# Kernel optimization log

Measured on AMD Instinct MI355X. Metric: run time of the kernel, lower is better.

Reference implementation:

```python
import jax, jax.numpy as jnp
import numpy as np

USER_NUM = 100_000
ITEM_NUM = 50_000
N = USER_NUM + ITEM_NUM          # total nodes in the bipartite graph
HIDDEN = 64
LAYERS = 3
BATCH = 4096
NNZ = 4_800_000                  # ~avg degree 32


def setup_inputs() -> dict:
    key = jax.random.key(0)
    ks = jax.random.split(key, 7)
    emb = jax.random.normal(ks[0], (N, HIDDEN), dtype=jnp.float32) * 0.02
    rows = jax.random.randint(ks[1], (NNZ,), 0, N, dtype=jnp.int32)
    cols = jax.random.randint(ks[2], (NNZ,), 0, N, dtype=jnp.int32)
    # normalized-laplacian-like positive values, scaled ~ 1/avg_degree
    vals = jax.random.uniform(ks[3], (NNZ,), dtype=jnp.float32) * (1.0 / 32.0)
    user = jax.random.randint(ks[4], (BATCH,), 0, USER_NUM, dtype=jnp.int32)
    pos = jax.random.randint(ks[5], (BATCH,), USER_NUM, N, dtype=jnp.int32)
    neg = jax.random.randint(ks[6], (BATCH,), USER_NUM, N, dtype=jnp.int32)
    return {"emb": emb, "vals": vals, "rows": rows, "cols": cols,
            "user": user, "pos": pos, "neg": neg}


def _spmm(rows, cols, vals, x):
    # sparse [N,N] @ dense [N,d] in COO form: gather + scale + segment-sum
    return jax.ops.segment_sum(vals[:, None] * x[cols], rows, num_segments=N)


def reference(emb, vals, rows, cols, user, pos, neg):
    # layer-0 gathers
    user_acc = emb[user]
    pos_acc = emb[pos]
    neg_acc = emb[neg]
    e = emb
    for _ in range(LAYERS):
        e = _spmm(rows, cols, vals, e)
        user_acc = user_acc + e[user]
        pos_acc = pos_acc + e[pos]
        neg_acc = neg_acc + e[neg]
    denom = jnp.float32(LAYERS + 1)
    u = user_acc / denom   # mean over stacked layers
    p = pos_acc / denom
    n = neg_acc / denom
    pos_logits = jnp.einsum('id,id->i', u, p)
    neg_logits = jnp.einsum('id,id->i', u, n)
    # -log(sigmoid(x)) == -log_sigmoid(x) (numerically stable)
    loss = -jax.nn.log_sigmoid(pos_logits - neg_logits)
    return loss.sum()
```

## Files before the change

### kernel.cpp

```cpp
#include <hip/hip_runtime.h>

#define HIDDEN 64
#define PAD 96
#define CHUNK 8192
#define NBMAX 640
#define CAP 9600
#define S_SCALE 64.0f
#define INV_S 0.015625f

typedef unsigned int uint;
typedef unsigned char uchar;

__device__ __forceinline__ ushort f2bf(float f) {
    uint u = __float_as_uint(f);
    u = (u + 0x7FFFu + ((u >> 16) & 1u)) >> 16;
    return (ushort)u;
}
__device__ __forceinline__ float bf2f(ushort h) {
    return __uint_as_float(((uint)h) << 16);
}

#if __has_builtin(__builtin_amdgcn_cvt_pk_fp8_f32) && __has_builtin(__builtin_amdgcn_cvt_pk_f32_fp8)
#define FP8_HW 1
#else
#define FP8_HW 0
#endif

__device__ __forceinline__ uint enc8(float a, float b, float c, float d) {
#if FP8_HW
    int r = __builtin_amdgcn_cvt_pk_fp8_f32(a, b, 0, false);
    r = __builtin_amdgcn_cvt_pk_fp8_f32(c, d, r, true);
    return (uint)r;
#else
    auto enc1 = [](float x) -> uint {
        uint u = __float_as_uint(x);
        uint s = (u >> 24) & 0x80u;
        float af = fabsf(x);
        if (af < 0.015625f) return s;
        if (af >= 448.f) return s | 0x7Eu;
        uint bits = u & 0x7FFFFFFFu;
        bits -= (120u << 23);
        uint r = (bits + 0x7FFFFu + ((bits >> 20) & 1u)) >> 20;
        if (r > 0x7Eu) r = 0x7Eu;
        return s | r;
    };
    return enc1(a) | (enc1(b) << 8) | (enc1(c) << 16) | (enc1(d) << 24);
#endif
}

__device__ __forceinline__ float4 dec8(uint u) {
#if FP8_HW
    auto lo = __builtin_amdgcn_cvt_pk_f32_fp8((int)u, false);
    auto hi = __builtin_amdgcn_cvt_pk_f32_fp8((int)u, true);
    return make_float4(lo[0], lo[1], hi[0], hi[1]);
#else
    auto dec1 = [](uint b) -> float {
        uint m = b & 0x7Fu;
        uint s = (b & 0x80u) << 24;
        uint bits = m ? (s | ((m + 960u) << 20)) : s;
        return __uint_as_float(bits);
    };
    return make_float4(dec1(u & 0xFF), dec1((u >> 8) & 0xFF),
                       dec1((u >> 16) & 0xFF), dec1((u >> 24) & 0xFF));
#endif
}


__global__ void __launch_bounds__(256) k_f2fp8(const float4* __restrict__ src,
                                               uint2* __restrict__ dst, int n8) {
    int i = blockIdx.x * blockDim.x + threadIdx.x;
    if (i >= n8) return;
    float4 f0 = src[2 * i], f1 = src[2 * i + 1];
    uint2 o;
    o.x = enc8(f0.x * S_SCALE, f0.y * S_SCALE, f0.z * S_SCALE, f0.w * S_SCALE);
    o.y = enc8(f1.x * S_SCALE, f1.y * S_SCALE, f1.z * S_SCALE, f1.w * S_SCALE);
    dst[i] = o;
}


__global__ void __launch_bounds__(1024) k_stage(const int* __restrict__ rows,
                                                const int* __restrict__ cols,
                                                const float* __restrict__ vals,
                                                int* __restrict__ cursor,
                                                uint* __restrict__ smeta,
                                                ushort* __restrict__ sval,
                                                int nnz, int nb) {
    __shared__ int    hS[NBMAX];
    __shared__ int    lsS[NBMAX];
    __shared__ int    gsS[NBMAX];
    __shared__ int    lcS[NBMAX];
    __shared__ int    ps[1024];
    __shared__ uint   stgm[CHUNK];
    __shared__ ushort stgv[CHUNK];

    int t  = threadIdx.x;
    int cb = blockIdx.x * CHUNK;

    for (int k = t; k < nb; k += 1024) hS[k] = 0;
    __syncthreads();

    int4 ra[2];
    #pragma unroll
    for (int j = 0; j < 2; ++j) {
        int idx = cb + j * 4096 + t * 4;
        int4 r4;
        if (idx + 3 < nnz) {
            r4 = *(const int4*)(rows + idx);
        } else {
            r4.x = (idx     < nnz) ? rows[idx]     : -1;
            r4.y = (idx + 1 < nnz) ? rows[idx + 1] : -1;
            r4.z = (idx + 2 < nnz) ? rows[idx + 2] : -1;
            r4.w = (idx + 3 < nnz) ? rows[idx + 3] : -1;
        }
        ra[j] = r4;
        if (r4.x >= 0) atomicAdd(&hS[r4.x >> 8], 1);
        if (r4.y >= 0) atomicAdd(&hS[r4.y >> 8], 1);
        if (r4.z >= 0) atomicAdd(&hS[r4.z >> 8], 1);
        if (r4.w >= 0) atomicAdd(&hS[r4.w >> 8], 1);
    }
    __syncthreads();

    int k0 = 2 * t, k1 = 2 * t + 1;
    int c0 = (k0 < nb) ? hS[k0] : 0;
    int c1 = (k1 < nb) ? hS[k1] : 0;
    ps[t] = c0 + c1;
    __syncthreads();
    for (int d = 1; d < 1024; d <<= 1) {
        int p = (t >= d) ? ps[t - d] : 0;
        __syncthreads();
        ps[t] += p;
        __syncthreads();
    }
    int excl = ps[t] - (c0 + c1);
    if (k0 < nb) { lsS[k0] = excl;      gsS[k0] = atomicAdd(&cursor[k0], c0); }
    if (k1 < nb) { lsS[k1] = excl + c0; gsS[k1] = atomicAdd(&cursor[k1], c1); }
    __syncthreads();
    for (int k = t; k < nb; k += 1024) lcS[k] = lsS[k];
    __syncthreads();

    #pragma unroll
    for (int j = 0; j < 2; ++j) {
        int idx = cb + j * 4096 + t * 4;
        int4 r4 = ra[j];
        int4 c4; float4 v4;
        if (idx + 3 < nnz) {
            c4 = *(const int4*)(cols + idx);
            v4 = *(const float4*)(vals + idx);
        } else {
            c4.x = (idx     < nnz) ? cols[idx]     : 0;
            c4.y = (idx + 1 < nnz) ? cols[idx + 1] : 0;
            c4.z = (idx + 2 < nnz) ? cols[idx + 2] : 0;
            c4.w = (idx + 3 < nnz) ? cols[idx + 3] : 0;
            v4.x = (idx     < nnz) ? vals[idx]     : 0.f;
            v4.y = (idx + 1 < nnz) ? vals[idx + 1] : 0.f;
            v4.z = (idx + 2 < nnz) ? vals[idx + 2] : 0.f;
            v4.w = (idx + 3 < nnz) ? vals[idx + 3] : 0.f;
        }
        if (r4.x >= 0) { int s = atomicAdd(&lcS[r4.x >> 8], 1);
            stgm[s] = (uint)c4.x | ((uint)(r4.x & 255) << 18); stgv[s] = f2bf(v4.x); }
        if (r4.y >= 0) { int s = atomicAdd(&lcS[r4.y >> 8], 1);
            stgm[s] = (uint)c4.y | ((uint)(r4.y & 255) << 18); stgv[s] = f2bf(v4.y); }
        if (r4.z >= 0) { int s = atomicAdd(&lcS[r4.z >> 8], 1);
            stgm[s] = (uint)c4.z | ((uint)(r4.z & 255) << 18); stgv[s] = f2bf(v4.z); }
        if (r4.w >= 0) { int s = atomicAdd(&lcS[r4.w >> 8], 1);
            stgm[s] = (uint)c4.w | ((uint)(r4.w & 255) << 18); stgv[s] = f2bf(v4.w); }
    }
    __syncthreads();

    int m_total = nnz - cb; if (m_total > CHUNK) m_total = CHUNK;
    for (int i = t; i < m_total; i += 1024) {
        int lo = 0, hi = nb - 1;
        while (lo < hi) {
            int mid = (lo + hi + 1) >> 1;
            if (lsS[mid] <= i) lo = mid; else hi = mid - 1;
        }
        int k = lo;
        int pos = gsS[k] + (i - lsS[k]);
        if (pos < CAP) {
            smeta[(size_t)k * CAP + pos] = stgm[i];
            sval [(size_t)k * CAP + pos] = stgv[i];
        }
    }
}

__global__ void __launch_bounds__(1024) k_fine(const uint* __restrict__ smeta,
                                               const ushort* __restrict__ sval,
                                               const int* __restrict__ stagecnt,
                                               int* __restrict__ cols_ell,
                                               ushort* __restrict__ vals_ell,
                                               int* __restrict__ cnt, int n) {
    __shared__ uint   out_m[CAP];
    __shared__ ushort out_v[CAP];
    __shared__ int hist[256], rstart[256], cursor[256], s2[256];
    int k = blockIdx.x;
    int t = threadIdx.x;
    size_t s0 = (size_t)k * CAP;
    int ck = stagecnt[k]; if (ck > CAP) ck = CAP;
    if (t < 256) hist[t] = 0;
    __syncthreads();
    for (int i = t; i < ck; i += 1024)
        atomicAdd(&hist[smeta[s0 + i] >> 18], 1);
    __syncthreads();
    if (t < 256) s2[t] = hist[t];
    __syncthreads();
    for (int d = 1; d < 256; d <<= 1) {
        int p = (t < 256 && t >= d) ? s2[t - d] : 0;
        __syncthreads();
        if (t < 256) s2[t] += p;
        __syncthreads();
    }
    if (t < 256) {
        int rs = s2[t] - hist[t];
        rstart[t] = rs;
        cursor[t] = rs;
        int row = (k << 8) + t;
        if (row < n) cnt[row] = hist[t];
    }
    __syncthreads();
    for (int i = t; i < ck; i += 1024) {
        uint m = smeta[s0 + i];
        ushort v = sval[s0 + i];
        int lr = (int)(m >> 18);
        int slot = atomicAdd(&cursor[lr], 1);
        if (slot < CAP) { out_m[slot] = m & 0x3FFFFu; out_v[slot] = v; }
    }
    __syncthreads();
    for (int idx = t; idx < 256 * PAD; idx += 1024) {
        int lr = idx / PAD, j = idx - lr * PAD;
        if (j < hist[lr]) {
            int row = (k << 8) + lr;
            cols_ell[(size_t)row * PAD + j] = (int)out_m[rstart[lr] + j];
            vals_ell[(size_t)row * PAD + j] = out_v[rstart[lr] + j];
        }
    }
}


__device__ __forceinline__ float4 spmm_row4(const int* __restrict__ cnt,
                                            const int* __restrict__ cols_ell,
                                            const ushort* __restrict__ vals_ell,
                                            const uchar* __restrict__ x,
                                            int row, int lane) {
    int len = cnt[row]; if (len > PAD) len = PAD;
    const int*    cbp = cols_ell + (size_t)row * PAD;
    const ushort* vbp = vals_ell + (size_t)row * PAD;
    int g4 = (lane & 15) * 4;
    int e = lane >> 4;
    float a0 = 0.f, a1 = 0.f, a2 = 0.f, a3 = 0.f;
    float b0 = 0.f, b1 = 0.f, b2 = 0.f, b3 = 0.f;
    for (int j0 = 0; j0 < len; j0 += 64) {
        int m = len - j0; if (m > 64) m = 64;
        int c = 0; float v = 0.f;
        if (lane < m) {
            c = cbp[j0 + lane];
            v = bf2f(vbp[j0 + lane]);
        }
        int steps = (m + 3) >> 2;
        int s = 0;
        for (; s + 3 < steps; s += 4) {
            int i0 = 4 * s + e, i1 = i0 + 4, i2 = i0 + 8, i3 = i0 + 12;
            int   c0 = __shfl(c, i0); int   c1 = __shfl(c, i1);
            int   c2 = __shfl(c, i2); int   c3 = __shfl(c, i3);
            float v0 = __shfl(v, i0); float v1 = __shfl(v, i1);
            float v2 = __shfl(v, i2); float v3 = __shfl(v, i3);
            uint u0 = *(const uint*)(x + ((size_t)c0 << 6) + g4);
            uint u1 = *(const uint*)(x + ((size_t)c1 << 6) + g4);
            uint u2 = *(const uint*)(x + ((size_t)c2 << 6) + g4);
            uint u3 = *(const uint*)(x + ((size_t)c3 << 6) + g4);
            float4 x0 = dec8(u0); float4 x1 = dec8(u1);
            float4 x2 = dec8(u2); float4 x3 = dec8(u3);
            a0 += v0 * x0.x; a1 += v0 * x0.y; a2 += v0 * x0.z; a3 += v0 * x0.w;
            b0 += v1 * x1.x; b1 += v1 * x1.y; b2 += v1 * x1.z; b3 += v1 * x1.w;
            a0 += v2 * x2.x; a1 += v2 * x2.y; a2 += v2 * x2.z; a3 += v2 * x2.w;
            b0 += v3 * x3.x; b1 += v3 * x3.y; b2 += v3 * x3.z; b3 += v3 * x3.w;
        }
        for (; s < steps; ++s) {
            int i0 = 4 * s + e;
            int c0 = __shfl(c, i0); float v0 = __shfl(v, i0);
            uint u0 = *(const uint*)(x + ((size_t)c0 << 6) + g4);
            float4 x0 = dec8(u0);
            a0 += v0 * x0.x; a1 += v0 * x0.y; a2 += v0 * x0.z; a3 += v0 * x0.w;
        }
    }
    a0 += b0; a1 += b1; a2 += b2; a3 += b3;
    a0 += __shfl_xor(a0, 16); a1 += __shfl_xor(a1, 16);
    a2 += __shfl_xor(a2, 16); a3 += __shfl_xor(a3, 16);
    a0 += __shfl_xor(a0, 32); a1 += __shfl_xor(a1, 32);
    a2 += __shfl_xor(a2, 32); a3 += __shfl_xor(a3, 32);
    return make_float4(a0, a1, a2, a3);
}

__global__ void __launch_bounds__(256) k_spmm(const int* __restrict__ cnt,
                                              const int* __restrict__ cols_ell,
                                              const ushort* __restrict__ vals_ell,
                                              const uchar* __restrict__ x,
                                              uchar* __restrict__ y, int n) {
    int row  = (int)((blockIdx.x * blockDim.x + threadIdx.x) >> 6);
    int lane = threadIdx.x & 63;
    if (row >= n) return;
    float4 a = spmm_row4(cnt, cols_ell, vals_ell, x, row, lane);
    if (lane < 16) {
        uint r = enc8(a.x, a.y, a.z, a.w);
        *(uint*)(y + ((size_t)row << 6) + lane * 4) = r;
    }
}

__global__ void __launch_bounds__(256) k_spmm_batch(const int* __restrict__ cnt,
                                                    const int* __restrict__ cols_ell,
                                                    const ushort* __restrict__ vals_ell,
                                                    const uchar* __restrict__ x,
                                                    const int* __restrict__ user,
                                                    const int* __restrict__ pos,
                                                    const int* __restrict__ neg,
                                                    int batch, float* __restrict__ acc) {
    int slot = (int)((blockIdx.x * blockDim.x + threadIdx.x) >> 6);
    int lane = threadIdx.x & 63;
    if (slot >= 3 * batch) return;
    int which = slot / batch, i = slot - which * batch;
    const int* sel = (which == 0) ? user : (which == 1 ? pos : neg);
    float4 a = spmm_row4(cnt, cols_ell, vals_ell, x, sel[i], lane);
    if (lane < 16) {
        float4* p = (float4*)(acc + (size_t)slot * HIDDEN + lane * 4);
        float4 old = *p;
        old.x += a.x * INV_S; old.y += a.y * INV_S;
        old.z += a.z * INV_S; old.w += a.w * INV_S;
        *p = old;
    }
}


__global__ void __launch_bounds__(256) k_gather0(const float* __restrict__ e,
                                                 const int* __restrict__ user,
                                                 const int* __restrict__ pos,
                                                 const int* __restrict__ neg,
                                                 int batch, float* __restrict__ acc) {
    int row  = (int)((blockIdx.x * blockDim.x + threadIdx.x) >> 6);
    int lane = threadIdx.x & 63;
    if (row >= 3 * batch) return;
    int which = row / batch, i = row - which * batch;
    const int* sel = (which == 0) ? user : (which == 1 ? pos : neg);
    int s = sel[i];
    acc[(size_t)row * HIDDEN + lane] = e[(size_t)s * HIDDEN + lane];
}

__global__ void __launch_bounds__(256) k_gather8(const uchar* __restrict__ e,
                                                 const int* __restrict__ user,
                                                 const int* __restrict__ pos,
                                                 const int* __restrict__ neg,
                                                 int batch, float* __restrict__ acc) {
    int t    = blockIdx.x * blockDim.x + threadIdx.x;
    int wv   = t >> 6;
    int lane = threadIdx.x & 63;
    int row  = wv * 4 + (lane >> 4);
    if (row >= 3 * batch) return;
    int which = row / batch, i = row - which * batch;
    const int* sel = (which == 0) ? user : (which == 1 ? pos : neg);
    int s = sel[i];
    int g4 = (lane & 15) * 4;
    uint u = *(const uint*)(e + ((size_t)s << 6) + g4);
    float4 d = dec8(u);
    float4* p = (float4*)(acc + (size_t)row * HIDDEN + g4);
    float4 old = *p;
    old.x += d.x * INV_S; old.y += d.y * INV_S;
    old.z += d.z * INV_S; old.w += d.w * INV_S;
    *p = old;
}


__global__ void __launch_bounds__(256) k_loss(const float* __restrict__ acc, int batch,
                                              float* __restrict__ out) {
    int i    = (int)((blockIdx.x * blockDim.x + threadIdx.x) >> 6);
    int lane = threadIdx.x & 63;
    if (i >= batch) return;
    float u  = acc[(size_t)i * HIDDEN + lane] * 0.25f;
    float p  = acc[(size_t)(i + batch) * HIDDEN + lane] * 0.25f;
    float nn = acc[(size_t)(i + 2 * batch) * HIDDEN + lane] * 0.25f;
    float sp = u * p, sn = u * nn;
    for (int d = 32; d > 0; d >>= 1) {
        sp += __shfl_down(sp, d);
        sn += __shfl_down(sn, d);
    }
    if (lane == 0) {
        float z = sn - sp;
        float loss = fmaxf(z, 0.f) + log1pf(expf(-fabsf(z)));
        atomicAdd(out, loss);
    }
}


extern "C" void kernel_launch(void* const* d_in, const int* in_sizes, int n_in,
                              void* d_out, int out_size, void* d_ws, size_t ws_size,
                              hipStream_t stream) {
    (void)n_in; (void)out_size; (void)ws_size;
    const float* emb  = (const float*)d_in[0];
    const float* vals = (const float*)d_in[1];
    const int*   rows = (const int*)d_in[2];
    const int*   cols = (const int*)d_in[3];
    const int*   user = (const int*)d_in[4];
    const int*   pos  = (const int*)d_in[5];
    const int*   neg  = (const int*)d_in[6];

    const int n     = in_sizes[0] / HIDDEN;
    const int nnz   = in_sizes[1];
    const int batch = in_sizes[4];

    const int nb   = (n + 255) >> 8;
    const int nblk = (nnz + CHUNK - 1) / CHUNK;

    auto align256 = [](size_t x) { return (x + 255) & ~(size_t)255; };
    char* w = (char*)d_ws;
    int*    cnt      = (int*)w;    w += align256(sizeof(int)    * (size_t)n);
    int*    cursor   = (int*)w;    w += align256(sizeof(int)    * (size_t)NBMAX);
    int*    cols_ell = (int*)w;    w += align256(sizeof(int)    * (size_t)n * PAD);
    ushort* vals_ell = (ushort*)w; w += align256(sizeof(ushort) * (size_t)n * PAD);
    uchar*  emb8     = (uchar*)w;  w += align256((size_t)n * HIDDEN);
    uchar*  e0       = (uchar*)w;  w += align256((size_t)n * HIDDEN);
    uchar*  e1       = (uchar*)w;  w += align256((size_t)n * HIDDEN);
    float*  acc      = (float*)w;  w += align256(sizeof(float)  * (size_t)3 * batch * HIDDEN);
    uint*   smeta    = (uint*)w;   w += align256(sizeof(uint)   * (size_t)nb * CAP);
    ushort* sval     = (ushort*)w; w += align256(sizeof(ushort) * (size_t)nb * CAP);

    float* out = (float*)d_out;

    const int B = 256;
    dim3 blk(B);
    int g_conv = (n * HIDDEN / 8 + B - 1) / B;
    int g_spmm = (n + 3) / 4;
    int g_gath = (3 * batch + 3) / 4;
    int g_g8   = ((3 * batch + 3) / 4 * 64 + B - 1) / B;
    int g_loss = (batch + 3) / 4;

    hipMemsetAsync(cursor, 0, sizeof(int) * (size_t)NBMAX, stream);
    k_stage<<<nblk, 1024, 0, stream>>>(rows, cols, vals, cursor, smeta, sval, nnz, nb);
    k_fine<<<nb, 1024, 0, stream>>>(smeta, sval, cursor, cols_ell, vals_ell, cnt, n);

    k_f2fp8<<<g_conv, blk, 0, stream>>>((const float4*)emb, (uint2*)emb8, n * HIDDEN / 8);

    hipMemsetAsync(out, 0, sizeof(float), stream);

    k_gather0<<<g_gath, blk, 0, stream>>>(emb, user, pos, neg, batch, acc);
    k_spmm<<<g_spmm, blk, 0, stream>>>(cnt, cols_ell, vals_ell, emb8, e0, n);
    k_gather8<<<g_g8, blk, 0, stream>>>(e0, user, pos, neg, batch, acc);
    k_spmm<<<g_spmm, blk, 0, stream>>>(cnt, cols_ell, vals_ell, e0, e1, n);
    k_gather8<<<g_g8, blk, 0, stream>>>(e1, user, pos, neg, batch, acc);
    k_spmm_batch<<<g_gath, blk, 0, stream>>>(cnt, cols_ell, vals_ell, e1, user, pos, neg, batch, acc);

    k_loss<<<g_loss, blk, 0, stream>>>(acc, batch, out);
}
```

Measured before the change: 304.7 us.

## Pack ELL column and value into one word and split SpMM rows by halves

The staging kernel records each entry's bucket index in shared memory, which replaces the per-element binary search during scatter. The ELL format now packs an 18-bit column and a 14-bit truncated bf16 value into a single uint, padded to multiples of 16. This removes the separate value array and the shuffle-based broadcast in the SpMM inner loop. SpMM now gives each wave half of the 64 hidden features for a row, with lanes splitting entries eight ways, and blocks are ordered so both halves of the same rows run close together. Values lose two more mantissa bits, and each row's index list is read by two waves instead of one.

```diff
diff --git a/kernel.cpp b/kernel.cpp
--- a/kernel.cpp
+++ b/kernel.cpp
@@ -92,6 +92,7 @@
     __shared__ int    ps[1024];
     __shared__ uint   stgm[CHUNK];
     __shared__ ushort stgv[CHUNK];
+    __shared__ ushort stgb[CHUNK];
 
     int t  = threadIdx.x;
     int cb = blockIdx.x * CHUNK;
@@ -156,25 +157,20 @@
             v4.z = (idx + 2 < nnz) ? vals[idx + 2] : 0.f;
             v4.w = (idx + 3 < nnz) ? vals[idx + 3] : 0.f;
         }
-        if (r4.x >= 0) { int s = atomicAdd(&lcS[r4.x >> 8], 1);
-            stgm[s] = (uint)c4.x | ((uint)(r4.x & 255) << 18); stgv[s] = f2bf(v4.x); }
-        if (r4.y >= 0) { int s = atomicAdd(&lcS[r4.y >> 8], 1);
-            stgm[s] = (uint)c4.y | ((uint)(r4.y & 255) << 18); stgv[s] = f2bf(v4.y); }
-        if (r4.z >= 0) { int s = atomicAdd(&lcS[r4.z >> 8], 1);
-            stgm[s] = (uint)c4.z | ((uint)(r4.z & 255) << 18); stgv[s] = f2bf(v4.z); }
-        if (r4.w >= 0) { int s = atomicAdd(&lcS[r4.w >> 8], 1);
-            stgm[s] = (uint)c4.w | ((uint)(r4.w & 255) << 18); stgv[s] = f2bf(v4.w); }
+        if (r4.x >= 0) { int k = r4.x >> 8; int s = atomicAdd(&lcS[k], 1);
+            stgm[s] = (uint)c4.x | ((uint)(r4.x & 255) << 18); stgv[s] = f2bf(v4.x); stgb[s] = (ushort)k; }
+        if (r4.y >= 0) { int k = r4.y >> 8; int s = atomicAdd(&lcS[k], 1);
+            stgm[s] = (uint)c4.y | ((uint)(r4.y & 255) << 18); stgv[s] = f2bf(v4.y); stgb[s] = (ushort)k; }
+        if (r4.z >= 0) { int k = r4.z >> 8; int s = atomicAdd(&lcS[k], 1);
+            stgm[s] = (uint)c4.z | ((uint)(r4.z & 255) << 18); stgv[s] = f2bf(v4.z); stgb[s] = (ushort)k; }
+        if (r4.w >= 0) { int k = r4.w >> 8; int s = atomicAdd(&lcS[k], 1);
+            stgm[s] = (uint)c4.w | ((uint)(r4.w & 255) << 18); stgv[s] = f2bf(v4.w); stgb[s] = (ushort)k; }
     }
     __syncthreads();
 
     int m_total = nnz - cb; if (m_total > CHUNK) m_total = CHUNK;
     for (int i = t; i < m_total; i += 1024) {
-        int lo = 0, hi = nb - 1;
-        while (lo < hi) {
-            int mid = (lo + hi + 1) >> 1;
-            if (lsS[mid] <= i) lo = mid; else hi = mid - 1;
-        }
-        int k = lo;
+        int k = stgb[i];
         int pos = gsS[k] + (i - lsS[k]);
         if (pos < CAP) {
             smeta[(size_t)k * CAP + pos] = stgm[i];
@@ -186,11 +182,9 @@
 __global__ void __launch_bounds__(1024) k_fine(const uint* __restrict__ smeta,
                                                const ushort* __restrict__ sval,
                                                const int* __restrict__ stagecnt,
-                                               int* __restrict__ cols_ell,
-                                               ushort* __restrict__ vals_ell,
+                                               uint* __restrict__ ell,
                                                int* __restrict__ cnt, int n) {
-    __shared__ uint   out_m[CAP];
-    __shared__ ushort out_v[CAP];
+    __shared__ uint out_m[CAP];
     __shared__ int hist[256], rstart[256], cursor[256], s2[256];
     int k = blockIdx.x;
     int t = threadIdx.x;
@@ -219,70 +213,57 @@
     __syncthreads();
     for (int i = t; i < ck; i += 1024) {
         uint m = smeta[s0 + i];
-        ushort v = sval[s0 + i];
+        uint v = (uint)sval[s0 + i];
         int lr = (int)(m >> 18);
         int slot = atomicAdd(&cursor[lr], 1);
-        if (slot < CAP) { out_m[slot] = m & 0x3FFFFu; out_v[slot] = v; }
+        uint v14 = (v + 2u) >> 2;
+        if (v14 > 0x3FFFu) v14 = 0x3FFFu;
+        if (slot < CAP) out_m[slot] = (m & 0x3FFFFu) | (v14 << 18);
     }
     __syncthreads();
     for (int idx = t; idx < 256 * PAD; idx += 1024) {
         int lr = idx / PAD, j = idx - lr * PAD;
-        if (j < hist[lr]) {
+        int cr = hist[lr];
+        int cr16 = (cr + 15) & ~15;
+        if (j < cr) {
             int row = (k << 8) + lr;
-            cols_ell[(size_t)row * PAD + j] = (int)out_m[rstart[lr] + j];
-            vals_ell[(size_t)row * PAD + j] = out_v[rstart[lr] + j];
+            ell[(size_t)row * PAD + j] = out_m[rstart[lr] + j];
+        } else if (j < cr16) {
+            int row = (k << 8) + lr;
+            ell[(size_t)row * PAD + j] = 0u;
         }
     }
 }
 
 
-__device__ __forceinline__ float4 spmm_row4(const int* __restrict__ cnt,
-                                            const int* __restrict__ cols_ell,
-                                            const ushort* __restrict__ vals_ell,
-                                            const uchar* __restrict__ x,
-                                            int row, int lane) {
+__device__ __forceinline__ float4 spmm_row_half(const int* __restrict__ cnt,
+                                                const uint* __restrict__ ell,
+                                                const uchar* __restrict__ x,
+                                                int row, int lane, int half) {
     int len = cnt[row]; if (len > PAD) len = PAD;
-    const int*    cbp = cols_ell + (size_t)row * PAD;
-    const ushort* vbp = vals_ell + (size_t)row * PAD;
-    int g4 = (lane & 15) * 4;
-    int e = lane >> 4;
+    int len16 = (len + 15) & ~15;
+    const uint* mbp = ell + (size_t)row * PAD;
+    int e  = lane >> 3;
+    int g4 = (lane & 7) * 4 + half * 32;
     float a0 = 0.f, a1 = 0.f, a2 = 0.f, a3 = 0.f;
     float b0 = 0.f, b1 = 0.f, b2 = 0.f, b3 = 0.f;
-    for (int j0 = 0; j0 < len; j0 += 64) {
-        int m = len - j0; if (m > 64) m = 64;
-        int c = 0; float v = 0.f;
-        if (lane < m) {
-            c = cbp[j0 + lane];
-            v = bf2f(vbp[j0 + lane]);
-        }
-        int steps = (m + 3) >> 2;
-        int s = 0;
-        for (; s + 3 < steps; s += 4) {
-            int i0 = 4 * s + e, i1 = i0 + 4, i2 = i0 + 8, i3 = i0 + 12;
-            int   c0 = __shfl(c, i0); int   c1 = __shfl(c, i1);
-            int   c2 = __shfl(c, i2); int   c3 = __shfl(c, i3);
-            float v0 = __shfl(v, i0); float v1 = __shfl(v, i1);
-            float v2 = __shfl(v, i2); float v3 = __shfl(v, i3);
-            uint u0 = *(const uint*)(x + ((size_t)c0 << 6) + g4);
-            uint u1 = *(const uint*)(x + ((size_t)c1 << 6) + g4);
-            uint u2 = *(const uint*)(x + ((size_t)c2 << 6) + g4);
-            uint u3 = *(const uint*)(x + ((size_t)c3 << 6) + g4);
-            float4 x0 = dec8(u0); float4 x1 = dec8(u1);
-            float4 x2 = dec8(u2); float4 x3 = dec8(u3);
-            a0 += v0 * x0.x; a1 += v0 * x0.y; a2 += v0 * x0.z; a3 += v0 * x0.w;
-            b0 += v1 * x1.x; b1 += v1 * x1.y; b2 += v1 * x1.z; b3 += v1 * x1.w;
-            a0 += v2 * x2.x; a1 += v2 * x2.y; a2 += v2 * x2.z; a3 += v2 * x2.w;
-            b0 += v3 * x3.x; b1 += v3 * x3.y; b2 += v3 * x3.z; b3 += v3 * x3.w;
-        }
-        for (; s < steps; ++s) {
-            int i0 = 4 * s + e;
-            int c0 = __shfl(c, i0); float v0 = __shfl(v, i0);
-            uint u0 = *(const uint*)(x + ((size_t)c0 << 6) + g4);
-            float4 x0 = dec8(u0);
-            a0 += v0 * x0.x; a1 += v0 * x0.y; a2 += v0 * x0.z; a3 += v0 * x0.w;
-        }
+    for (int j = 0; j < len16; j += 16) {
+        uint m0 = mbp[j + e];
+        uint m1 = mbp[j + 8 + e];
+        int   c0 = (int)(m0 & 0x3FFFFu);
+        int   c1 = (int)(m1 & 0x3FFFFu);
+        float v0 = bf2f((ushort)((m0 >> 18) << 2));
+        float v1 = bf2f((ushort)((m1 >> 18) << 2));
+        uint u0 = *(const uint*)(x + ((size_t)c0 << 6) + g4);
+        uint u1 = *(const uint*)(x + ((size_t)c1 << 6) + g4);
+        float4 x0 = dec8(u0);
+        float4 x1 = dec8(u1);
+        a0 += v0 * x0.x; a1 += v0 * x0.y; a2 += v0 * x0.z; a3 += v0 * x0.w;
+        b0 += v1 * x1.x; b1 += v1 * x1.y; b2 += v1 * x1.z; b3 += v1 * x1.w;
     }
     a0 += b0; a1 += b1; a2 += b2; a3 += b3;
+    a0 += __shfl_xor(a0, 8);  a1 += __shfl_xor(a1, 8);
+    a2 += __shfl_xor(a2, 8);  a3 += __shfl_xor(a3, 8);
     a0 += __shfl_xor(a0, 16); a1 += __shfl_xor(a1, 16);
     a2 += __shfl_xor(a2, 16); a3 += __shfl_xor(a3, 16);
     a0 += __shfl_xor(a0, 32); a1 += __shfl_xor(a1, 32);
@@ -291,36 +272,40 @@
 }
 
 __global__ void __launch_bounds__(256) k_spmm(const int* __restrict__ cnt,
-                                              const int* __restrict__ cols_ell,
-                                              const ushort* __restrict__ vals_ell,
+                                              const uint* __restrict__ ell,
                                               const uchar* __restrict__ x,
                                               uchar* __restrict__ y, int n) {
-    int row  = (int)((blockIdx.x * blockDim.x + threadIdx.x) >> 6);
+    int b = blockIdx.x;
+    int q = b >> 3, r = b & 7;
+    int half = r >> 2;
+    int row = (q * 4 + (r & 3)) * 4 + (int)(threadIdx.x >> 6);
     int lane = threadIdx.x & 63;
     if (row >= n) return;
-    float4 a = spmm_row4(cnt, cols_ell, vals_ell, x, row, lane);
-    if (lane < 16) {
-        uint r = enc8(a.x, a.y, a.z, a.w);
-        *(uint*)(y + ((size_t)row << 6) + lane * 4) = r;
+    float4 a = spmm_row_half(cnt, ell, x, row, lane, half);
+    if (lane < 8) {
+        uint o = enc8(a.x, a.y, a.z, a.w);
+        *(uint*)(y + ((size_t)row << 6) + half * 32 + lane * 4) = o;
     }
 }
 
 __global__ void __launch_bounds__(256) k_spmm_batch(const int* __restrict__ cnt,
-                                                    const int* __restrict__ cols_ell,
-                                                    const ushort* __restrict__ vals_ell,
+                                                    const uint* __restrict__ ell,
                                                     const uchar* __restrict__ x,
                                                     const int* __restrict__ user,
                                                     const int* __restrict__ pos,
                                                     const int* __restrict__ neg,
                                                     int batch, float* __restrict__ acc) {
-    int slot = (int)((blockIdx.x * blockDim.x + threadIdx.x) >> 6);
+    int b = blockIdx.x;
+    int q = b >> 3, r = b & 7;
+    int half = r >> 2;
+    int slot = (q * 4 + (r & 3)) * 4 + (int)(threadIdx.x >> 6);
     int lane = threadIdx.x & 63;
     if (slot >= 3 * batch) return;
     int which = slot / batch, i = slot - which * batch;
     const int* sel = (which == 0) ? user : (which == 1 ? pos : neg);
-    float4 a = spmm_row4(cnt, cols_ell, vals_ell, x, sel[i], lane);
-    if (lane < 16) {
-        float4* p = (float4*)(acc + (size_t)slot * HIDDEN + lane * 4);
+    float4 a = spmm_row_half(cnt, ell, x, sel[i], lane, half);
+    if (lane < 8) {
+        float4* p = (float4*)(acc + (size_t)slot * HIDDEN + half * 32 + lane * 4);
         float4 old = *p;
         old.x += a.x * INV_S; old.y += a.y * INV_S;
         old.z += a.z * INV_S; old.w += a.w * INV_S;
@@ -409,41 +394,44 @@
 
     auto align256 = [](size_t x) { return (x + 255) & ~(size_t)255; };
     char* w = (char*)d_ws;
-    int*    cnt      = (int*)w;    w += align256(sizeof(int)    * (size_t)n);
-    int*    cursor   = (int*)w;    w += align256(sizeof(int)    * (size_t)NBMAX);
-    int*    cols_ell = (int*)w;    w += align256(sizeof(int)    * (size_t)n * PAD);
-    ushort* vals_ell = (ushort*)w; w += align256(sizeof(ushort) * (size_t)n * PAD);
-    uchar*  emb8     = (uchar*)w;  w += align256((size_t)n * HIDDEN);
-    uchar*  e0       = (uchar*)w;  w += align256((size_t)n * HIDDEN);
-    uchar*  e1       = (uchar*)w;  w += align256((size_t)n * HIDDEN);
-    float*  acc      = (float*)w;  w += align256(sizeof(float)  * (size_t)3 * batch * HIDDEN);
-    uint*   smeta    = (uint*)w;   w += align256(sizeof(uint)   * (size_t)nb * CAP);
-    ushort* sval     = (ushort*)w; w += align256(sizeof(ushort) * (size_t)nb * CAP);
+    int*    cnt    = (int*)w;    w += align256(sizeof(int)    * (size_t)n);
+    int*    cursor = (int*)w;    w += align256(sizeof(int)    * (size_t)NBMAX);
+    uint*   ell    = (uint*)w;   w += align256(sizeof(uint)   * (size_t)n * PAD);
+    uchar*  emb8   = (uchar*)w;  w += align256((size_t)n * HIDDEN);
+    uchar*  e0     = (uchar*)w;  w += align256((size_t)n * HIDDEN);
+    uchar*  e1     = (uchar*)w;  w += align256((size_t)n * HIDDEN);
+    float*  acc    = (float*)w;  w += align256(sizeof(float)  * (size_t)3 * batch * HIDDEN);
+    uint*   smeta  = (uint*)w;   w += align256(sizeof(uint)   * (size_t)nb * CAP);
+    ushort* sval   = (ushort*)w; w += align256(sizeof(ushort) * (size_t)nb * CAP);
 
     float* out = (float*)d_out;
 
     const int B = 256;
     dim3 blk(B);
     int g_conv = (n * HIDDEN / 8 + B - 1) / B;
-    int g_spmm = (n + 3) / 4;
+    int g_spmm = 2 * (((n + 3) / 4 + 3) / 4) * 4;
+    int G4 = ((n + 15) / 16);
+    g_spmm = G4 * 8;
+    int GB4 = ((3 * batch + 15) / 16);
+    int g_spmmb = GB4 * 8;
     int g_gath = (3 * batch + 3) / 4;
     int g_g8   = ((3 * batch + 3) / 4 * 64 + B - 1) / B;
     int g_loss = (batch + 3) / 4;
 
     hipMemsetAsync(cursor, 0, sizeof(int) * (size_t)NBMAX, stream);
     k_stage<<<nblk, 1024, 0, stream>>>(rows, cols, vals, cursor, smeta, sval, nnz, nb);
-    k_fine<<<nb, 1024, 0, stream>>>(smeta, sval, cursor, cols_ell, vals_ell, cnt, n);
+    k_fine<<<nb, 1024, 0, stream>>>(smeta, sval, cursor, ell, cnt, n);
 
     k_f2fp8<<<g_conv, blk, 0, stream>>>((const float4*)emb, (uint2*)emb8, n * HIDDEN / 8);
 
     hipMemsetAsync(out, 0, sizeof(float), stream);
 
     k_gather0<<<g_gath, blk, 0, stream>>>(emb, user, pos, neg, batch, acc);
-    k_spmm<<<g_spmm, blk, 0, stream>>>(cnt, cols_ell, vals_ell, emb8, e0, n);
+    k_spmm<<<g_spmm, blk, 0, stream>>>(cnt, ell, emb8, e0, n);
     k_gather8<<<g_g8, blk, 0, stream>>>(e0, user, pos, neg, batch, acc);
-    k_spmm<<<g_spmm, blk, 0, stream>>>(cnt, cols_ell, vals_ell, e0, e1, n);
+    k_spmm<<<g_spmm, blk, 0, stream>>>(cnt, ell, e0, e1, n);
     k_gather8<<<g_g8, blk, 0, stream>>>(e1, user, pos, neg, batch, acc);
-    k_spmm_batch<<<g_gath, blk, 0, stream>>>(cnt, cols_ell, vals_ell, e1, user, pos, neg, batch, acc);
+    k_spmm_batch<<<g_spmmb, blk, 0, stream>>>(cnt, ell, e1, user, pos, neg, batch, acc);
 
     k_loss<<<g_loss, blk, 0, stream>>>(acc, batch, out);
 }
```

After: 413.5 us. 1.36x slower.
